# Kernel tuning notes

Measured on AMD Instinct MI355X. Metric: run time of the kernel, lower is better.

Reference implementation:

```python
import jax, jax.numpy as jnp
import numpy as np


def sparsemax(z):
    """Euclidean projection onto the simplex (Martins & Astudillo 2016).
    z: (..., L) logits -> sparse probability vectors of same shape.
    """
    L = z.shape[-1]
    z_sorted = jnp.flip(jnp.sort(z, axis=-1), axis=-1)          # descending
    cum = jnp.cumsum(z_sorted, axis=-1)
    k = jnp.arange(1, L + 1, dtype=z.dtype)                     # 1..L
    support = 1.0 + k * z_sorted > cum                          # prefix-true mask
    k_max = jnp.sum(support, axis=-1, keepdims=True).astype(z.dtype)
    # sum of z_sorted over the support == cumsum at the last supported index
    cum_at_k = jnp.sum(jnp.where(support, z_sorted, 0.0), axis=-1, keepdims=True)
    tau = (cum_at_k - 1.0) / k_max
    return jnp.maximum(z - tau, 0.0)


def setup_inputs() -> dict:
    key = jax.random.key(0)
    k1, k2 = jax.random.split(key)
    B, K, L = 64, 16, 16384
    attention_logits = jax.random.normal(k1, (B, K, L), dtype=jnp.float32)
    rationale_mask = (jax.random.uniform(k2, (B, L)) < 0.1).astype(jnp.float32)
    return {"attention_logits": attention_logits, "rationale_mask": rationale_mask}


def reference(attention_logits, rationale_mask):
    # normalize the rationale mask into a probability target q
    q = rationale_mask / jnp.clip(
        jnp.sum(rationale_mask, axis=-1, keepdims=True), 1e-12, None
    )  # (B, L)
    p = sparsemax(attention_logits)            # (B, K, L), all heads batched
    diff = p - q[:, None, :]                   # broadcast target over heads
    # per-(example, head) loss 0.5*||p - q||^2, then mean over batch and heads
    # (= mean over heads of per-head batch means, as in the torch loop)
    return 0.5 * jnp.mean(jnp.sum(diff * diff, axis=-1))
```

## Files before the change

### kernel.cpp

```cpp
#include <hip/hip_runtime.h>

#define BB 64
#define KK 16
#define LL 16384
#define CAP 2048
#define NROW (BB * KK)

__global__ __launch_bounds__(256) void mask_stats_kernel(
    const float* __restrict__ mask, float* __restrict__ stats) {
  int b = blockIdx.x;
  const float* m = mask + (size_t)b * LL;
  int t = threadIdx.x;
  float s = 0.f, sq = 0.f;
#pragma unroll
  for (int j = 0; j < 16; ++j) {
    float4 v = reinterpret_cast<const float4*>(m)[j * 256 + t];
    s  += v.x + v.y + v.z + v.w;
    sq += v.x * v.x + v.y * v.y + v.z * v.z + v.w * v.w;
  }
  for (int off = 32; off; off >>= 1) {
    s  += __shfl_xor(s, off);
    sq += __shfl_xor(sq, off);
  }
  __shared__ float ls[4], lsq[4];
  int wave = t >> 6;
  if ((t & 63) == 0) { ls[wave] = s; lsq[wave] = sq; }
  __syncthreads();
  if (t == 0) {
    float S  = ls[0] + ls[1] + ls[2] + ls[3];
    float SQ = lsq[0] + lsq[1] + lsq[2] + lsq[3];
    float inv = 1.0f / fmaxf(S, 1e-12f);
    stats[2 * b]     = inv;
    stats[2 * b + 1] = SQ * inv * inv;
  }
}

__global__ __launch_bounds__(256, 4) void sparsemax_loss_kernel(
    const float* __restrict__ logits, const float* __restrict__ mask,
    float* __restrict__ ws) {
  int row = blockIdx.x;
  int b = row >> 4;
  const float* z = logits + (size_t)row * LL;
  const float* m = mask + (size_t)b * LL;
  const float4* zv = reinterpret_cast<const float4*>(z);
  int t = threadIdx.x;
  int wave = t >> 6, lane = t & 63;

  __shared__ float lds_val[CAP];
  __shared__ int   lds_idx[CAP];
  __shared__ int   lds_n;
  __shared__ float lds_f[4];

  if (t == 0) lds_n = 0;

  float4 v[16];
#pragma unroll
  for (int j = 0; j < 16; ++j) v[j] = zv[j * 256 + t];

  float mx0 = -3.0e38f, mx1 = -3.0e38f, mx2 = -3.0e38f, mx3 = -3.0e38f;
#pragma unroll
  for (int j = 0; j < 4; ++j) {
    mx0 = fmaxf(mx0, fmaxf(fmaxf(v[4*j+0].x, v[4*j+0].y), fmaxf(v[4*j+0].z, v[4*j+0].w)));
    mx1 = fmaxf(mx1, fmaxf(fmaxf(v[4*j+1].x, v[4*j+1].y), fmaxf(v[4*j+1].z, v[4*j+1].w)));
    mx2 = fmaxf(mx2, fmaxf(fmaxf(v[4*j+2].x, v[4*j+2].y), fmaxf(v[4*j+2].z, v[4*j+2].w)));
    mx3 = fmaxf(mx3, fmaxf(fmaxf(v[4*j+3].x, v[4*j+3].y), fmaxf(v[4*j+3].z, v[4*j+3].w)));
  }
  float vmax = fmaxf(fmaxf(mx0, mx1), fmaxf(mx2, mx3));
  for (int off = 32; off; off >>= 1) vmax = fmaxf(vmax, __shfl_xor(vmax, off));
  if (lane == 0) lds_f[wave] = vmax;
  __syncthreads();
  float zmax = fmaxf(fmaxf(lds_f[0], lds_f[1]), fmaxf(lds_f[2], lds_f[3]));
  float thr = zmax - 1.0f;

#pragma unroll
  for (int j = 0; j < 16; ++j) {
    int base = (j * 256 + t) * 4;
    float vv[4] = {v[j].x, v[j].y, v[j].z, v[j].w};
#pragma unroll
    for (int e = 0; e < 4; ++e) {
      if (vv[e] > thr) {
        int pos = atomicAdd(&lds_n, 1);
        if (pos < CAP) { lds_val[pos] = vv[e]; lds_idx[pos] = base + e; }
      }
    }
  }
  __syncthreads();
  int n = lds_n;

  if (n <= 64) {
    if (wave == 0) {
      float c = (lane < n) ? lds_val[lane] : -3.0e38f;
#pragma unroll
      for (int size = 2; size <= 64; size <<= 1) {
#pragma unroll
        for (int stride = size >> 1; stride > 0; stride >>= 1) {
          float other = __shfl_xor(c, stride);
          bool dirDesc = ((lane & size) == 0);
          bool takeMax = (dirDesc == ((lane & stride) == 0));
          float mn = fminf(c, other), mxv = fmaxf(c, other);
          c = takeMax ? mxv : mn;
        }
      }
      float cum = c;
#pragma unroll
      for (int off = 1; off < 64; off <<= 1) {
        float y = __shfl_up(cum, off);
        if (lane >= off) cum += y;
      }
      bool sup = (lane < n) && (1.0f + (float)(lane + 1) * c > cum);
      unsigned long long bal = __ballot(sup);
      int k = __popcll(bal);
      float S = sup ? c : 0.f;
      for (int off = 32; off; off >>= 1) S += __shfl_xor(S, off);
      float tau = (S - 1.0f) / (float)k;

      float a1 = 0.f, a2 = 0.f;
      if (lane < n) {
        float val = lds_val[lane];
        float p = fmaxf(val - tau, 0.f);
        if (p > 0.f) {
          a1 = p * p;
          a2 = p * m[lds_idx[lane]];
        }
      }
      for (int off = 32; off; off >>= 1) {
        a1 += __shfl_xor(a1, off);
        a2 += __shfl_xor(a2, off);
      }
      if (lane == 0) { ws[2 * row] = a1; ws[2 * row + 1] = a2; }
    }
  } else if (n <= CAP) {
    if (wave == 0) {
      int nj = (n + 63) >> 6;
      float lo = thr, hi = zmax;
      for (int it = 0; it < 30; ++it) {
        float mid = 0.5f * (lo + hi);
        float s = 0.f;
        for (int j = 0; j < nj; ++j) {
          int i = j * 64 + lane;
          float cc = (i < n) ? lds_val[i] : -3.0e38f;
          s += fmaxf(cc - mid, 0.f);
        }
        for (int off = 32; off; off >>= 1) s += __shfl_xor(s, off);
        if (s >= 1.0f) lo = mid; else hi = mid;
      }
      float S = 0.f, kc = 0.f;
      for (int j = 0; j < nj; ++j) {
        int i = j * 64 + lane;
        float cc = (i < n) ? lds_val[i] : -3.0e38f;
        if (cc > lo) { S += cc; kc += 1.f; }
      }
      for (int off = 32; off; off >>= 1) {
        S  += __shfl_xor(S, off);
        kc += __shfl_xor(kc, off);
      }
      float tau = (S - 1.0f) / kc;

      float a1 = 0.f, a2 = 0.f;
      for (int j = 0; j < nj; ++j) {
        int i = j * 64 + lane;
        if (i < n) {
          float p = fmaxf(lds_val[i] - tau, 0.f);
          if (p > 0.f) {
            a1 += p * p;
            a2 += p * m[lds_idx[i]];
          }
        }
      }
      for (int off = 32; off; off >>= 1) {
        a1 += __shfl_xor(a1, off);
        a2 += __shfl_xor(a2, off);
      }
      if (lane == 0) { ws[2 * row] = a1; ws[2 * row + 1] = a2; }
    }
  } else {
    __shared__ float red[4], red2[4];
    float lo = thr, hi = zmax;
    for (int it = 0; it < 30; ++it) {
      float mid = 0.5f * (lo + hi);
      float s = 0.f;
      for (int j = 0; j < 16; ++j) {
        float4 vv = zv[j * 256 + t];
        s += fmaxf(vv.x - mid, 0.f) + fmaxf(vv.y - mid, 0.f) +
             fmaxf(vv.z - mid, 0.f) + fmaxf(vv.w - mid, 0.f);
      }
      for (int off = 32; off; off >>= 1) s += __shfl_xor(s, off);
      __syncthreads();
      if (lane == 0) red[wave] = s;
      __syncthreads();
      float tot = red[0] + red[1] + red[2] + red[3];
      if (tot >= 1.0f) lo = mid; else hi = mid;
    }
    float S = 0.f, kc = 0.f;
    for (int j = 0; j < 16; ++j) {
      float4 vv4 = zv[j * 256 + t];
      float vv[4] = {vv4.x, vv4.y, vv4.z, vv4.w};
      for (int e = 0; e < 4; ++e)
        if (vv[e] > lo) { S += vv[e]; kc += 1.f; }
    }
    for (int off = 32; off; off >>= 1) {
      S  += __shfl_xor(S, off);
      kc += __shfl_xor(kc, off);
    }
    __syncthreads();
    if (lane == 0) { red[wave] = S; red2[wave] = kc; }
    __syncthreads();
    S  = red[0] + red[1] + red[2] + red[3];
    kc = red2[0] + red2[1] + red2[2] + red2[3];
    float tau = (S - 1.0f) / kc;

    float a1 = 0.f, a2 = 0.f;
    for (int j = 0; j < 16; ++j) {
      int base = (j * 256 + t) * 4;
      float4 vv4 = zv[j * 256 + t];
      float vv[4] = {vv4.x, vv4.y, vv4.z, vv4.w};
      for (int e = 0; e < 4; ++e) {
        float p = fmaxf(vv[e] - tau, 0.f);
        if (p > 0.f) {
          a1 += p * p;
          a2 += p * m[base + e];
        }
      }
    }
    for (int off = 32; off; off >>= 1) {
      a1 += __shfl_xor(a1, off);
      a2 += __shfl_xor(a2, off);
    }
    __syncthreads();
    if (lane == 0) { red[wave] = a1; red2[wave] = a2; }
    __syncthreads();
    if (t == 0) {
      a1 = red[0] + red[1] + red[2] + red[3];
      a2 = red2[0] + red2[1] + red2[2] + red2[3];
      ws[2 * row] = a1;
      ws[2 * row + 1] = a2;
    }
  }
}

__global__ __launch_bounds__(64) void combine_kernel(
    const float* __restrict__ ws, const float* __restrict__ stats,
    float* __restrict__ out) {
  int t = threadIdx.x;
  float inv   = stats[2 * t];
  float sumq2 = stats[2 * t + 1];
  float acc = 16.0f * sumq2;
#pragma unroll
  for (int kk = 0; kk < 16; ++kk) {
    float A1 = ws[2 * (t * 16 + kk)];
    float T2 = ws[2 * (t * 16 + kk) + 1];
    acc += A1 - 2.0f * inv * T2;
  }
  for (int off = 32; off; off >>= 1) acc += __shfl_xor(acc, off);
  if (t == 0) out[0] = acc * (0.5f / (float)(BB * KK));
}

extern "C" void kernel_launch(void* const* d_in, const int* in_sizes, int n_in,
                              void* d_out, int out_size, void* d_ws, size_t ws_size,
                              hipStream_t stream) {
  const float* logits = (const float*)d_in[0];
  const float* mask   = (const float*)d_in[1];
  float* ws    = (float*)d_ws;
  float* stats = (float*)d_ws + 2 * NROW;
  float* out   = (float*)d_out;

  mask_stats_kernel<<<BB, 256, 0, stream>>>(mask, stats);
  sparsemax_loss_kernel<<<NROW, 256, 0, stream>>>(logits, mask, ws);
  combine_kernel<<<1, 64, 0, stream>>>(ws, stats, out);
}
```

Baseline: 110.9 us.

## Fuse mask stats, sparsemax loss and combine into one kernel with last-block reduction

Merges the three kernel launches into a single grid where extra blocks compute the per-example mask statistics and the last block to finish, found through a global atomic counter, performs the final reduction. This removes two kernel launch overheads and the serialization gaps between them. In exchange it adds a global atomic and threadfence per block plus a device-global counter that must reset correctly between calls.

```diff
diff --git a/kernel.cpp b/kernel.cpp
--- a/kernel.cpp
+++ b/kernel.cpp
@@ -5,165 +5,198 @@
 #define LL 16384
 #define CAP 2048
 #define NROW (BB * KK)
-
-__global__ __launch_bounds__(256) void mask_stats_kernel(
-    const float* __restrict__ mask, float* __restrict__ stats) {
-  int b = blockIdx.x;
-  const float* m = mask + (size_t)b * LL;
-  int t = threadIdx.x;
-  float s = 0.f, sq = 0.f;
-#pragma unroll
-  for (int j = 0; j < 16; ++j) {
-    float4 v = reinterpret_cast<const float4*>(m)[j * 256 + t];
-    s  += v.x + v.y + v.z + v.w;
-    sq += v.x * v.x + v.y * v.y + v.z * v.z + v.w * v.w;
-  }
-  for (int off = 32; off; off >>= 1) {
-    s  += __shfl_xor(s, off);
-    sq += __shfl_xor(sq, off);
-  }
-  __shared__ float ls[4], lsq[4];
-  int wave = t >> 6;
-  if ((t & 63) == 0) { ls[wave] = s; lsq[wave] = sq; }
-  __syncthreads();
-  if (t == 0) {
-    float S  = ls[0] + ls[1] + ls[2] + ls[3];
-    float SQ = lsq[0] + lsq[1] + lsq[2] + lsq[3];
-    float inv = 1.0f / fmaxf(S, 1e-12f);
-    stats[2 * b]     = inv;
-    stats[2 * b + 1] = SQ * inv * inv;
-  }
-}
-
-__global__ __launch_bounds__(256, 4) void sparsemax_loss_kernel(
+#define NBLK (NROW + BB)
+
+__device__ unsigned int g_done = 0;
+
+__global__ __launch_bounds__(256, 4) void fused_all(
     const float* __restrict__ logits, const float* __restrict__ mask,
-    float* __restrict__ ws) {
+    float* __restrict__ ws, float* __restrict__ out) {
   int row = blockIdx.x;
-  int b = row >> 4;
-  const float* z = logits + (size_t)row * LL;
-  const float* m = mask + (size_t)b * LL;
-  const float4* zv = reinterpret_cast<const float4*>(z);
   int t = threadIdx.x;
   int wave = t >> 6, lane = t & 63;
+  float* stats = ws + 2 * NROW;
 
   __shared__ float lds_val[CAP];
   __shared__ int   lds_idx[CAP];
   __shared__ int   lds_n;
   __shared__ float lds_f[4];
-
-  if (t == 0) lds_n = 0;
-
-  float4 v[16];
-#pragma unroll
-  for (int j = 0; j < 16; ++j) v[j] = zv[j * 256 + t];
-
-  float mx0 = -3.0e38f, mx1 = -3.0e38f, mx2 = -3.0e38f, mx3 = -3.0e38f;
-#pragma unroll
-  for (int j = 0; j < 4; ++j) {
-    mx0 = fmaxf(mx0, fmaxf(fmaxf(v[4*j+0].x, v[4*j+0].y), fmaxf(v[4*j+0].z, v[4*j+0].w)));
-    mx1 = fmaxf(mx1, fmaxf(fmaxf(v[4*j+1].x, v[4*j+1].y), fmaxf(v[4*j+1].z, v[4*j+1].w)));
-    mx2 = fmaxf(mx2, fmaxf(fmaxf(v[4*j+2].x, v[4*j+2].y), fmaxf(v[4*j+2].z, v[4*j+2].w)));
-    mx3 = fmaxf(mx3, fmaxf(fmaxf(v[4*j+3].x, v[4*j+3].y), fmaxf(v[4*j+3].z, v[4*j+3].w)));
-  }
-  float vmax = fmaxf(fmaxf(mx0, mx1), fmaxf(mx2, mx3));
-  for (int off = 32; off; off >>= 1) vmax = fmaxf(vmax, __shfl_xor(vmax, off));
-  if (lane == 0) lds_f[wave] = vmax;
-  __syncthreads();
-  float zmax = fmaxf(fmaxf(lds_f[0], lds_f[1]), fmaxf(lds_f[2], lds_f[3]));
-  float thr = zmax - 1.0f;
-
-#pragma unroll
-  for (int j = 0; j < 16; ++j) {
-    int base = (j * 256 + t) * 4;
-    float vv[4] = {v[j].x, v[j].y, v[j].z, v[j].w};
-#pragma unroll
-    for (int e = 0; e < 4; ++e) {
-      if (vv[e] > thr) {
-        int pos = atomicAdd(&lds_n, 1);
-        if (pos < CAP) { lds_val[pos] = vv[e]; lds_idx[pos] = base + e; }
-      }
-    }
-  }
-  __syncthreads();
-  int n = lds_n;
-
-  if (n <= 64) {
-    if (wave == 0) {
-      float c = (lane < n) ? lds_val[lane] : -3.0e38f;
-#pragma unroll
-      for (int size = 2; size <= 64; size <<= 1) {
-#pragma unroll
-        for (int stride = size >> 1; stride > 0; stride >>= 1) {
-          float other = __shfl_xor(c, stride);
-          bool dirDesc = ((lane & size) == 0);
-          bool takeMax = (dirDesc == ((lane & stride) == 0));
-          float mn = fminf(c, other), mxv = fmaxf(c, other);
-          c = takeMax ? mxv : mn;
-        }
-      }
-      float cum = c;
-#pragma unroll
-      for (int off = 1; off < 64; off <<= 1) {
-        float y = __shfl_up(cum, off);
-        if (lane >= off) cum += y;
-      }
-      bool sup = (lane < n) && (1.0f + (float)(lane + 1) * c > cum);
-      unsigned long long bal = __ballot(sup);
-      int k = __popcll(bal);
-      float S = sup ? c : 0.f;
-      for (int off = 32; off; off >>= 1) S += __shfl_xor(S, off);
-      float tau = (S - 1.0f) / (float)k;
-
-      float a1 = 0.f, a2 = 0.f;
-      if (lane < n) {
-        float val = lds_val[lane];
-        float p = fmaxf(val - tau, 0.f);
-        if (p > 0.f) {
-          a1 = p * p;
-          a2 = p * m[lds_idx[lane]];
-        }
-      }
-      for (int off = 32; off; off >>= 1) {
-        a1 += __shfl_xor(a1, off);
-        a2 += __shfl_xor(a2, off);
-      }
-      if (lane == 0) { ws[2 * row] = a1; ws[2 * row + 1] = a2; }
-    }
-  } else if (n <= CAP) {
-    if (wave == 0) {
-      int nj = (n + 63) >> 6;
+  __shared__ int   lds_last;
+
+  if (row < NROW) {
+    int b = row >> 4;
+    const float* z = logits + (size_t)row * LL;
+    const float* m = mask + (size_t)b * LL;
+    const float4* zv = reinterpret_cast<const float4*>(z);
+
+    if (t == 0) lds_n = 0;
+
+    float4 v[16];
+#pragma unroll
+    for (int j = 0; j < 16; ++j) v[j] = zv[j * 256 + t];
+
+    float mx0 = -3.0e38f, mx1 = -3.0e38f, mx2 = -3.0e38f, mx3 = -3.0e38f;
+#pragma unroll
+    for (int j = 0; j < 4; ++j) {
+      mx0 = fmaxf(mx0, fmaxf(fmaxf(v[4*j+0].x, v[4*j+0].y), fmaxf(v[4*j+0].z, v[4*j+0].w)));
+      mx1 = fmaxf(mx1, fmaxf(fmaxf(v[4*j+1].x, v[4*j+1].y), fmaxf(v[4*j+1].z, v[4*j+1].w)));
+      mx2 = fmaxf(mx2, fmaxf(fmaxf(v[4*j+2].x, v[4*j+2].y), fmaxf(v[4*j+2].z, v[4*j+2].w)));
+      mx3 = fmaxf(mx3, fmaxf(fmaxf(v[4*j+3].x, v[4*j+3].y), fmaxf(v[4*j+3].z, v[4*j+3].w)));
+    }
+    float vmax = fmaxf(fmaxf(mx0, mx1), fmaxf(mx2, mx3));
+    for (int off = 32; off; off >>= 1) vmax = fmaxf(vmax, __shfl_xor(vmax, off));
+    if (lane == 0) lds_f[wave] = vmax;
+    __syncthreads();
+    float zmax = fmaxf(fmaxf(lds_f[0], lds_f[1]), fmaxf(lds_f[2], lds_f[3]));
+    float thr = zmax - 1.0f;
+
+#pragma unroll
+    for (int j = 0; j < 16; ++j) {
+      int base = (j * 256 + t) * 4;
+      float vv[4] = {v[j].x, v[j].y, v[j].z, v[j].w};
+#pragma unroll
+      for (int e = 0; e < 4; ++e) {
+        if (vv[e] > thr) {
+          int pos = atomicAdd(&lds_n, 1);
+          if (pos < CAP) { lds_val[pos] = vv[e]; lds_idx[pos] = base + e; }
+        }
+      }
+    }
+    __syncthreads();
+    int n = lds_n;
+
+    if (n <= 64) {
+      if (wave == 0) {
+        float c = (lane < n) ? lds_val[lane] : -3.0e38f;
+#pragma unroll
+        for (int size = 2; size <= 64; size <<= 1) {
+#pragma unroll
+          for (int stride = size >> 1; stride > 0; stride >>= 1) {
+            float other = __shfl_xor(c, stride);
+            bool dirDesc = ((lane & size) == 0);
+            bool takeMax = (dirDesc == ((lane & stride) == 0));
+            float mn = fminf(c, other), mxv = fmaxf(c, other);
+            c = takeMax ? mxv : mn;
+          }
+        }
+        float cum = c;
+#pragma unroll
+        for (int off = 1; off < 64; off <<= 1) {
+          float y = __shfl_up(cum, off);
+          if (lane >= off) cum += y;
+        }
+        bool sup = (lane < n) && (1.0f + (float)(lane + 1) * c > cum);
+        unsigned long long bal = __ballot(sup);
+        int k = __popcll(bal);
+        float S = sup ? c : 0.f;
+        for (int off = 32; off; off >>= 1) S += __shfl_xor(S, off);
+        float tau = (S - 1.0f) / (float)k;
+
+        float a1 = 0.f, a2 = 0.f;
+        if (lane < n) {
+          float val = lds_val[lane];
+          float p = fmaxf(val - tau, 0.f);
+          if (p > 0.f) {
+            a1 = p * p;
+            a2 = p * m[lds_idx[lane]];
+          }
+        }
+        for (int off = 32; off; off >>= 1) {
+          a1 += __shfl_xor(a1, off);
+          a2 += __shfl_xor(a2, off);
+        }
+        if (lane == 0) { ws[2 * row] = a1; ws[2 * row + 1] = a2; }
+      }
+    } else if (n <= CAP) {
+      if (wave == 0) {
+        int nj = (n + 63) >> 6;
+        float lo = thr, hi = zmax;
+        for (int it = 0; it < 30; ++it) {
+          float mid = 0.5f * (lo + hi);
+          float s = 0.f;
+          for (int j = 0; j < nj; ++j) {
+            int i = j * 64 + lane;
+            float cc = (i < n) ? lds_val[i] : -3.0e38f;
+            s += fmaxf(cc - mid, 0.f);
+          }
+          for (int off = 32; off; off >>= 1) s += __shfl_xor(s, off);
+          if (s >= 1.0f) lo = mid; else hi = mid;
+        }
+        float S = 0.f, kc = 0.f;
+        for (int j = 0; j < nj; ++j) {
+          int i = j * 64 + lane;
+          float cc = (i < n) ? lds_val[i] : -3.0e38f;
+          if (cc > lo) { S += cc; kc += 1.f; }
+        }
+        for (int off = 32; off; off >>= 1) {
+          S  += __shfl_xor(S, off);
+          kc += __shfl_xor(kc, off);
+        }
+        float tau = (S - 1.0f) / kc;
+
+        float a1 = 0.f, a2 = 0.f;
+        for (int j = 0; j < nj; ++j) {
+          int i = j * 64 + lane;
+          if (i < n) {
+            float p = fmaxf(lds_val[i] - tau, 0.f);
+            if (p > 0.f) {
+              a1 += p * p;
+              a2 += p * m[lds_idx[i]];
+            }
+          }
+        }
+        for (int off = 32; off; off >>= 1) {
+          a1 += __shfl_xor(a1, off);
+          a2 += __shfl_xor(a2, off);
+        }
+        if (lane == 0) { ws[2 * row] = a1; ws[2 * row + 1] = a2; }
+      }
+    } else {
+      __shared__ float red[4], red2[4];
       float lo = thr, hi = zmax;
       for (int it = 0; it < 30; ++it) {
         float mid = 0.5f * (lo + hi);
         float s = 0.f;
-        for (int j = 0; j < nj; ++j) {
-          int i = j * 64 + lane;
-          float cc = (i < n) ? lds_val[i] : -3.0e38f;
-          s += fmaxf(cc - mid, 0.f);
+        for (int j = 0; j < 16; ++j) {
+          float4 vv = zv[j * 256 + t];
+          s += fmaxf(vv.x - mid, 0.f) + fmaxf(vv.y - mid, 0.f) +
+               fmaxf(vv.z - mid, 0.f) + fmaxf(vv.w - mid, 0.f);
         }
         for (int off = 32; off; off >>= 1) s += __shfl_xor(s, off);
-        if (s >= 1.0f) lo = mid; else hi = mid;
+        __syncthreads();
+        if (lane == 0) red[wave] = s;
+        __syncthreads();
+        float tot = red[0] + red[1] + red[2] + red[3];
+        if (tot >= 1.0f) lo = mid; else hi = mid;
       }
       float S = 0.f, kc = 0.f;
-      for (int j = 0; j < nj; ++j) {
-        int i = j * 64 + lane;
-        float cc = (i < n) ? lds_val[i] : -3.0e38f;
-        if (cc > lo) { S += cc; kc += 1.f; }
+      for (int j = 0; j < 16; ++j) {
+        float4 vv4 = zv[j * 256 + t];
+        float vv[4] = {vv4.x, vv4.y, vv4.z, vv4.w};
+        for (int e = 0; e < 4; ++e)
+          if (vv[e] > lo) { S += vv[e]; kc += 1.f; }
       }
       for (int off = 32; off; off >>= 1) {
         S  += __shfl_xor(S, off);
         kc += __shfl_xor(kc, off);
       }
+      __syncthreads();
+      if (lane == 0) { red[wave] = S; red2[wave] = kc; }
+      __syncthreads();
+      S  = red[0] + red[1] + red[2] + red[3];
+      kc = red2[0] + red2[1] + red2[2] + red2[3];
       float tau = (S - 1.0f) / kc;
 
       float a1 = 0.f, a2 = 0.f;
-      for (int j = 0; j < nj; ++j) {
-        int i = j * 64 + lane;
-        if (i < n) {
-          float p = fmaxf(lds_val[i] - tau, 0.f);
+      for (int j = 0; j < 16; ++j) {
+        int base = (j * 256 + t) * 4;
+        float4 vv4 = zv[j * 256 + t];
+        float vv[4] = {vv4.x, vv4.y, vv4.z, vv4.w};
+        for (int e = 0; e < 4; ++e) {
+          float p = fmaxf(vv[e] - tau, 0.f);
           if (p > 0.f) {
             a1 += p * p;
-            a2 += p * m[lds_idx[i]];
+            a2 += p * m[base + e];
           }
         }
       }
@@ -171,88 +204,70 @@
         a1 += __shfl_xor(a1, off);
         a2 += __shfl_xor(a2, off);
       }
-      if (lane == 0) { ws[2 * row] = a1; ws[2 * row + 1] = a2; }
+      __syncthreads();
+      if (lane == 0) { red[wave] = a1; red2[wave] = a2; }
+      __syncthreads();
+      if (t == 0) {
+        a1 = red[0] + red[1] + red[2] + red[3];
+        a2 = red2[0] + red2[1] + red2[2] + red2[3];
+        ws[2 * row] = a1;
+        ws[2 * row + 1] = a2;
+      }
     }
   } else {
-    __shared__ float red[4], red2[4];
-    float lo = thr, hi = zmax;
-    for (int it = 0; it < 30; ++it) {
-      float mid = 0.5f * (lo + hi);
-      float s = 0.f;
-      for (int j = 0; j < 16; ++j) {
-        float4 vv = zv[j * 256 + t];
-        s += fmaxf(vv.x - mid, 0.f) + fmaxf(vv.y - mid, 0.f) +
-             fmaxf(vv.z - mid, 0.f) + fmaxf(vv.w - mid, 0.f);
-      }
-      for (int off = 32; off; off >>= 1) s += __shfl_xor(s, off);
-      __syncthreads();
-      if (lane == 0) red[wave] = s;
-      __syncthreads();
-      float tot = red[0] + red[1] + red[2] + red[3];
-      if (tot >= 1.0f) lo = mid; else hi = mid;
-    }
-    float S = 0.f, kc = 0.f;
+    int b = row - NROW;
+    const float* m = mask + (size_t)b * LL;
+    float s = 0.f, sq = 0.f;
+#pragma unroll
     for (int j = 0; j < 16; ++j) {
-      float4 vv4 = zv[j * 256 + t];
-      float vv[4] = {vv4.x, vv4.y, vv4.z, vv4.w};
-      for (int e = 0; e < 4; ++e)
-        if (vv[e] > lo) { S += vv[e]; kc += 1.f; }
+      float4 v = reinterpret_cast<const float4*>(m)[j * 256 + t];
+      s  += v.x + v.y + v.z + v.w;
+      sq += v.x * v.x + v.y * v.y + v.z * v.z + v.w * v.w;
     }
     for (int off = 32; off; off >>= 1) {
-      S  += __shfl_xor(S, off);
-      kc += __shfl_xor(kc, off);
-    }
-    __syncthreads();
-    if (lane == 0) { red[wave] = S; red2[wave] = kc; }
-    __syncthreads();
-    S  = red[0] + red[1] + red[2] + red[3];
-    kc = red2[0] + red2[1] + red2[2] + red2[3];
-    float tau = (S - 1.0f) / kc;
-
-    float a1 = 0.f, a2 = 0.f;
-    for (int j = 0; j < 16; ++j) {
-      int base = (j * 256 + t) * 4;
-      float4 vv4 = zv[j * 256 + t];
-      float vv[4] = {vv4.x, vv4.y, vv4.z, vv4.w};
-      for (int e = 0; e < 4; ++e) {
-        float p = fmaxf(vv[e] - tau, 0.f);
-        if (p > 0.f) {
-          a1 += p * p;
-          a2 += p * m[base + e];
-        }
-      }
-    }
-    for (int off = 32; off; off >>= 1) {
-      a1 += __shfl_xor(a1, off);
-      a2 += __shfl_xor(a2, off);
-    }
-    __syncthreads();
-    if (lane == 0) { red[wave] = a1; red2[wave] = a2; }
+      s  += __shfl_xor(s, off);
+      sq += __shfl_xor(sq, off);
+    }
+    __shared__ float ls[4], lsq[4];
+    if (lane == 0) { ls[wave] = s; lsq[wave] = sq; }
     __syncthreads();
     if (t == 0) {
-      a1 = red[0] + red[1] + red[2] + red[3];
-      a2 = red2[0] + red2[1] + red2[2] + red2[3];
-      ws[2 * row] = a1;
-      ws[2 * row + 1] = a2;
+      float S  = ls[0] + ls[1] + ls[2] + ls[3];
+      float SQ = lsq[0] + lsq[1] + lsq[2] + lsq[3];
+      float inv = 1.0f / fmaxf(S, 1e-12f);
+      stats[2 * b]     = inv;
+      stats[2 * b + 1] = SQ * inv * inv;
     }
   }
-}
-
-__global__ __launch_bounds__(64) void combine_kernel(
-    const float* __restrict__ ws, const float* __restrict__ stats,
-    float* __restrict__ out) {
-  int t = threadIdx.x;
-  float inv   = stats[2 * t];
-  float sumq2 = stats[2 * t + 1];
-  float acc = 16.0f * sumq2;
-#pragma unroll
-  for (int kk = 0; kk < 16; ++kk) {
-    float A1 = ws[2 * (t * 16 + kk)];
-    float T2 = ws[2 * (t * 16 + kk) + 1];
-    acc += A1 - 2.0f * inv * T2;
+
+  if (t == 0) {
+    __threadfence();
+    unsigned old = atomicAdd(&g_done, 1u);
+    int last = (old == NBLK - 1);
+    lds_last = last;
+    if (last) atomicExch(&g_done, 0u);
   }
-  for (int off = 32; off; off >>= 1) acc += __shfl_xor(acc, off);
-  if (t == 0) out[0] = acc * (0.5f / (float)(BB * KK));
+  __syncthreads();
+
+  if (lds_last) {
+    __threadfence();
+    float acc = 0.f;
+    if (t < 64) {
+      float inv   = stats[2 * t];
+      float sumq2 = stats[2 * t + 1];
+      acc = 16.0f * sumq2;
+#pragma unroll
+      for (int kk = 0; kk < 16; ++kk) {
+        float A1 = ws[2 * (t * 16 + kk)];
+        float T2 = ws[2 * (t * 16 + kk) + 1];
+        acc += A1 - 2.0f * inv * T2;
+      }
+    }
+    if (wave == 0) {
+      for (int off = 32; off; off >>= 1) acc += __shfl_xor(acc, off);
+      if (t == 0) out[0] = acc * (0.5f / (float)(BB * KK));
+    }
+  }
 }
 
 extern "C" void kernel_launch(void* const* d_in, const int* in_sizes, int n_in,
@@ -260,11 +275,8 @@
                               hipStream_t stream) {
   const float* logits = (const float*)d_in[0];
   const float* mask   = (const float*)d_in[1];
-  float* ws    = (float*)d_ws;
-  float* stats = (float*)d_ws + 2 * NROW;
-  float* out   = (float*)d_out;
-
-  mask_stats_kernel<<<BB, 256, 0, stream>>>(mask, stats);
-  sparsemax_loss_kernel<<<NROW, 256, 0, stream>>>(logits, mask, ws);
-  combine_kernel<<<1, 64, 0, stream>>>(ws, stats, out);
+  float* ws  = (float*)d_ws;
+  float* out = (float*)d_out;
+
+  fused_all<<<NBLK, 256, 0, stream>>>(logits, mask, ws, out);
 }
```

Result: slower. 126.1 us (+13.7%).
